# Performance work log

Hardware: AMD Instinct MI355X
Metric: run time of the kernel (lower is better)

Reference implementation:

```python
import jax, jax.numpy as jnp
import numpy as np


def setup_inputs() -> dict:
    key = jax.random.key(0)
    ks = jax.random.split(key, 6)
    B, N, D, Dm, Do = 4, 512, 64, 64, 64
    vertices = jax.random.normal(ks[0], (B, N, D), dtype=jnp.float32)
    mask = jax.random.randint(ks[1], (B, N), 0, 2).astype(bool)
    W_msg = jax.random.normal(ks[2], (Dm, 2 * D), dtype=jnp.float32) / np.sqrt(2 * D).astype(np.float32)
    b_msg = jnp.zeros((Dm,), dtype=jnp.float32)
    W_node = jax.random.normal(ks[3], (Do, D + Dm), dtype=jnp.float32) / np.sqrt(D + Dm).astype(np.float32)
    b_node = jnp.zeros((Do,), dtype=jnp.float32)
    return {"vertices": vertices, "mask": mask, "W_msg": W_msg, "b_msg": b_msg,
            "W_node": W_node, "b_node": b_node}


def reference(vertices, mask, W_msg, b_msg, W_node, b_node):
    # vertices: (B,N,D); mask: (B,N) bool
    D = vertices.shape[-1]
    # message_layer(cat(v_i, v_j)) == v_i @ Wi^T + v_j @ Wj^T + b  (split weight)
    Wi, Wj = W_msg[:, :D], W_msg[:, D:]
    a = jnp.einsum('bnd,md->bnm', vertices, Wi)   # (B,N,Dm) src-half
    c = jnp.einsum('bnd,md->bnm', vertices, Wj)   # (B,N,Dm) dst-half
    msg = jax.nn.relu(a[:, :, None, :] + c[:, None, :, :] + b_msg)  # (B,N,N,Dm)
    pair_mask = (mask[:, :, None] & mask[:, None, :])[..., None]    # (B,N,N,1)
    msg = jnp.where(pair_mask, msg, jnp.zeros((), msg.dtype))
    agg = msg.sum(axis=2)                                           # (B,N,Dm)
    h = jnp.concatenate([vertices, agg], axis=-1)                   # (B,N,D+Dm)
    out = jax.nn.relu(jnp.einsum('bnd,od->bno', h, W_node) + b_node)
    return out
```

## Files before the change

### kernel.cpp

```cpp
#include <hip/hip_runtime.h>


typedef float v2f __attribute__((ext_vector_type(2)));

__device__ __forceinline__ v2f pk_add(v2f a, v2f b) {
    v2f d;
    asm("v_pk_add_f32 %0, %1, %2" : "=v"(d) : "v"(a), "v"(b));
    return d;
}

__global__ __launch_bounds__(256) void prep3(
    const float* __restrict__ V, const int* __restrict__ mask,
    const float* __restrict__ Wmsg, const float* __restrict__ bmsg,
    const float* __restrict__ Wn, const float* __restrict__ bn,
    float* __restrict__ A, float* __restrict__ C, float* __restrict__ O1)
{
    __shared__ float wm_s[64 * 132];
    __shared__ float wn1_s[64 * 68];
    int tid = threadIdx.x;

#pragma unroll
    for (int k = 0; k < 8; ++k) {
        int f4 = tid + k * 256;
        int mm = f4 >> 5, dd = (f4 & 31) << 2;
        *(float4*)&wm_s[mm * 132 + dd] = ((const float4*)Wmsg)[f4];
    }
#pragma unroll
    for (int k = 0; k < 4; ++k) {
        int f4 = tid + k * 256;
        int oo = f4 >> 4, kk = (f4 & 15) << 2;
        *(float4*)&wn1_s[oo * 68 + kk] = *(const float4*)&Wn[oo * 128 + kk];
    }
    __syncthreads();

    int m  = tid & 63;
    int rq = tid >> 6;
    int row0 = __builtin_amdgcn_readfirstlane(blockIdx.x * 8 + rq * 2);
    const float* v0 = V + row0 * 64;
    const float* v1 = v0 + 64;

    float sa0 = bmsg[m], sa1 = sa0;
    float sc0 = 0.f, sc1 = 0.f;
    float so0 = bn[m], so1 = so0;
#pragma unroll
    for (int d0 = 0; d0 < 64; d0 += 4) {
        float4 wa = *(float4*)&wm_s[m * 132 + d0];
        float4 wc = *(float4*)&wm_s[m * 132 + 64 + d0];
        float4 wo = *(float4*)&wn1_s[m * 68 + d0];
        float4 va = *(const float4*)&v0[d0];
        float4 vb = *(const float4*)&v1[d0];
        sa0 = fmaf(va.x, wa.x, sa0); sa0 = fmaf(va.y, wa.y, sa0);
        sa0 = fmaf(va.z, wa.z, sa0); sa0 = fmaf(va.w, wa.w, sa0);
        sc0 = fmaf(va.x, wc.x, sc0); sc0 = fmaf(va.y, wc.y, sc0);
        sc0 = fmaf(va.z, wc.z, sc0); sc0 = fmaf(va.w, wc.w, sc0);
        so0 = fmaf(va.x, wo.x, so0); so0 = fmaf(va.y, wo.y, so0);
        so0 = fmaf(va.z, wo.z, so0); so0 = fmaf(va.w, wo.w, so0);
        sa1 = fmaf(vb.x, wa.x, sa1); sa1 = fmaf(vb.y, wa.y, sa1);
        sa1 = fmaf(vb.z, wa.z, sa1); sa1 = fmaf(vb.w, wa.w, sa1);
        sc1 = fmaf(vb.x, wc.x, sc1); sc1 = fmaf(vb.y, wc.y, sc1);
        sc1 = fmaf(vb.z, wc.z, sc1); sc1 = fmaf(vb.w, wc.w, sc1);
        so1 = fmaf(vb.x, wo.x, so1); so1 = fmaf(vb.y, wo.y, so1);
        so1 = fmaf(vb.z, wo.z, so1); so1 = fmaf(vb.w, wo.w, so1);
    }
    int mk0 = mask[row0], mk1 = mask[row0 + 1];
    A [row0 * 64 + m]       = sa0;
    A [(row0 + 1) * 64 + m] = sa1;
    C [row0 * 64 + m]       = mk0 ? sc0 : -1e30f;
    C [(row0 + 1) * 64 + m] = mk1 ? sc1 : -1e30f;
    O1[row0 * 64 + m]       = so0;
    O1[(row0 + 1) * 64 + m] = so1;
}

__global__ __launch_bounds__(1024) void agg3(
    const int* __restrict__ mask,
    const float* __restrict__ A, const float* __restrict__ C,
    const float* __restrict__ O1, const float* __restrict__ Wn,
    float* __restrict__ out)
{
    __shared__ float smem[8192];
    __shared__ float wn2_s[64 * 68];
    __shared__ float agg_s[8 * 64];

    int tid = threadIdx.x;
    int m  = tid & 63;
    int jc = tid >> 6;
    int i0 = blockIdx.x * 8;
    int b  = blockIdx.x >> 6;
    const float* cb = C + (size_t)b * 512 * 64;

    {
        int oo = tid >> 4, kk = (tid & 15) << 2;
        *(float4*)&wn2_s[oo * 68 + kk] = *(const float4*)&Wn[oo * 128 + 64 + kk];
    }

    v2f ad[8], acc[8];
#pragma unroll
    for (int r = 0; r < 8; ++r) {
        float a = A[(i0 + r) * 64 + m];
        ad[r]  = (v2f){a, a};
        acc[r] = (v2f){0.f, 0.f};
    }

    for (int j0 = 0; j0 < 512; j0 += 128) {
        __syncthreads();
        const float4* src = (const float4*)(cb + (size_t)j0 * 64);
        float4* dst = (float4*)smem;
        dst[tid]        = src[tid];
        dst[tid + 1024] = src[tid + 1024];
        __syncthreads();
        const float* cbase = smem + jc * 8 * 64 + m;
#pragma unroll
        for (int p = 0; p < 4; ++p) {
            v2f c2 = {cbase[p * 128], cbase[p * 128 + 64]};
#pragma unroll
            for (int r = 0; r < 8; ++r) {
                v2f x = pk_add(ad[r], c2);
                x.x = fmaxf(x.x, 0.f);
                x.y = fmaxf(x.y, 0.f);
                acc[r] = pk_add(acc[r], x);
            }
        }
    }
    __syncthreads();
#pragma unroll
    for (int r = 0; r < 8; ++r)
        smem[jc * 512 + r * 64 + m] = acc[r].x + acc[r].y;
    __syncthreads();

    if (tid < 512) {
        int r = tid >> 6;
        float aggsum = 0.f;
#pragma unroll
        for (int q = 0; q < 16; ++q) aggsum += smem[q * 512 + r * 64 + m];
        agg_s[r * 64 + m] = mask[i0 + r] ? aggsum : 0.f;
    }
    __syncthreads();
    if (tid < 512) {
        int r = tid >> 6;
        float s = O1[(i0 + r) * 64 + m];
#pragma unroll
        for (int k = 0; k < 64; k += 4) {
            float4 h4 = *(float4*)&agg_s[r * 64 + k];
            float4 w4 = *(float4*)&wn2_s[m * 68 + k];
            s = fmaf(h4.x, w4.x, s); s = fmaf(h4.y, w4.y, s);
            s = fmaf(h4.z, w4.z, s); s = fmaf(h4.w, w4.w, s);
        }
        out[(i0 + r) * 64 + m] = fmaxf(s, 0.f);
    }
}

extern "C" void kernel_launch(void* const* d_in, const int* in_sizes, int n_in,
                              void* d_out, int out_size, void* d_ws, size_t ws_size,
                              hipStream_t stream) {
    const float* V    = (const float*)d_in[0];
    const int*   mask = (const int*)d_in[1];
    const float* Wmsg = (const float*)d_in[2];
    const float* bmsg = (const float*)d_in[3];
    const float* Wn   = (const float*)d_in[4];
    const float* bn   = (const float*)d_in[5];
    float* outp = (float*)d_out;

    const int BN = in_sizes[1];
    float* A  = (float*)d_ws;
    float* Cc = A  + (size_t)BN * 64;
    float* O1 = Cc + (size_t)BN * 64;

    prep3<<<dim3(BN / 8), dim3(256),  0, stream>>>(V, mask, Wmsg, bmsg, Wn, bn, A, Cc, O1);
    agg3 <<<dim3(BN / 8), dim3(1024), 0, stream>>>(mask, A, Cc, O1, Wn, outp);
}
```

Measured before the change: 20.70 us.

## Fuse prep and aggregation kernels into one cooperative kernel with grid sync

```diff
diff --git a/kernel.cpp b/kernel.cpp
--- a/kernel.cpp
+++ b/kernel.cpp
@@ -1,4 +1,7 @@
 #include <hip/hip_runtime.h>
+#include <hip/hip_cooperative_groups.h>
+
+namespace cg = cooperative_groups;
 
 
 typedef float v2f __attribute__((ext_vector_type(2)));
@@ -9,106 +12,89 @@
     return d;
 }
 
-__global__ __launch_bounds__(256) void prep3(
+__global__ __launch_bounds__(1024) void fused_graphblock(
     const float* __restrict__ V, const int* __restrict__ mask,
     const float* __restrict__ Wmsg, const float* __restrict__ bmsg,
     const float* __restrict__ Wn, const float* __restrict__ bn,
-    float* __restrict__ A, float* __restrict__ C, float* __restrict__ O1)
+    float* __restrict__ C, float* __restrict__ out)
 {
-    __shared__ float wm_s[64 * 132];
-    __shared__ float wn1_s[64 * 68];
+    __shared__ float buf[12800];
+    __shared__ float a_s[512];
+    __shared__ float agg_s[512];
+
     int tid = threadIdx.x;
+    int i0  = blockIdx.x * 8;
+    int b   = blockIdx.x >> 6;
+
+    float* wm  = buf;
+    float* wn1 = buf + 8448;
 
 #pragma unroll
-    for (int k = 0; k < 8; ++k) {
-        int f4 = tid + k * 256;
+    for (int k = 0; k < 2; ++k) {
+        int f4 = tid + k * 1024;
         int mm = f4 >> 5, dd = (f4 & 31) << 2;
-        *(float4*)&wm_s[mm * 132 + dd] = ((const float4*)Wmsg)[f4];
+        *(float4*)&wm[mm * 132 + dd] = ((const float4*)Wmsg)[f4];
     }
-#pragma unroll
-    for (int k = 0; k < 4; ++k) {
-        int f4 = tid + k * 256;
-        int oo = f4 >> 4, kk = (f4 & 15) << 2;
-        *(float4*)&wn1_s[oo * 68 + kk] = *(const float4*)&Wn[oo * 128 + kk];
+    {
+        int oo = tid >> 4, kk = (tid & 15) << 2;
+        *(float4*)&wn1[oo * 68 + kk] = *(const float4*)&Wn[oo * 128 + kk];
     }
     __syncthreads();
 
-    int m  = tid & 63;
-    int rq = tid >> 6;
-    int row0 = __builtin_amdgcn_readfirstlane(blockIdx.x * 8 + rq * 2);
-    const float* v0 = V + row0 * 64;
-    const float* v1 = v0 + 64;
+    float o1 = 0.f;
+    int   mk = 0;
+    if (tid < 512) {
+        int m = tid & 63;
+        int row = __builtin_amdgcn_readfirstlane(i0 + (tid >> 6));
+        const float* v = V + row * 64;
+        float sa = bmsg[m], sc = 0.f, so = bn[m];
+#pragma unroll
+        for (int d0 = 0; d0 < 64; d0 += 4) {
+            float4 va = *(const float4*)&v[d0];
+            float4 wa = *(float4*)&wm[m * 132 + d0];
+            float4 wc = *(float4*)&wm[m * 132 + 64 + d0];
+            float4 wo = *(float4*)&wn1[m * 68 + d0];
+            sa = fmaf(va.x, wa.x, sa); sa = fmaf(va.y, wa.y, sa);
+            sa = fmaf(va.z, wa.z, sa); sa = fmaf(va.w, wa.w, sa);
+            sc = fmaf(va.x, wc.x, sc); sc = fmaf(va.y, wc.y, sc);
+            sc = fmaf(va.z, wc.z, sc); sc = fmaf(va.w, wc.w, sc);
+            so = fmaf(va.x, wo.x, so); so = fmaf(va.y, wo.y, so);
+            so = fmaf(va.z, wo.z, so); so = fmaf(va.w, wo.w, so);
+        }
+        mk = mask[row];
+        a_s[tid] = sa;
+        C[row * 64 + m] = mk ? sc : -1e30f;
+        o1 = so;
+    }
 
-    float sa0 = bmsg[m], sa1 = sa0;
-    float sc0 = 0.f, sc1 = 0.f;
-    float so0 = bn[m], so1 = so0;
-#pragma unroll
-    for (int d0 = 0; d0 < 64; d0 += 4) {
-        float4 wa = *(float4*)&wm_s[m * 132 + d0];
-        float4 wc = *(float4*)&wm_s[m * 132 + 64 + d0];
-        float4 wo = *(float4*)&wn1_s[m * 68 + d0];
-        float4 va = *(const float4*)&v0[d0];
-        float4 vb = *(const float4*)&v1[d0];
-        sa0 = fmaf(va.x, wa.x, sa0); sa0 = fmaf(va.y, wa.y, sa0);
-        sa0 = fmaf(va.z, wa.z, sa0); sa0 = fmaf(va.w, wa.w, sa0);
-        sc0 = fmaf(va.x, wc.x, sc0); sc0 = fmaf(va.y, wc.y, sc0);
-        sc0 = fmaf(va.z, wc.z, sc0); sc0 = fmaf(va.w, wc.w, sc0);
-        so0 = fmaf(va.x, wo.x, so0); so0 = fmaf(va.y, wo.y, so0);
-        so0 = fmaf(va.z, wo.z, so0); so0 = fmaf(va.w, wo.w, so0);
-        sa1 = fmaf(vb.x, wa.x, sa1); sa1 = fmaf(vb.y, wa.y, sa1);
-        sa1 = fmaf(vb.z, wa.z, sa1); sa1 = fmaf(vb.w, wa.w, sa1);
-        sc1 = fmaf(vb.x, wc.x, sc1); sc1 = fmaf(vb.y, wc.y, sc1);
-        sc1 = fmaf(vb.z, wc.z, sc1); sc1 = fmaf(vb.w, wc.w, sc1);
-        so1 = fmaf(vb.x, wo.x, so1); so1 = fmaf(vb.y, wo.y, so1);
-        so1 = fmaf(vb.z, wo.z, so1); so1 = fmaf(vb.w, wo.w, so1);
+    cg::this_grid().sync();
+
+    float* ctile = buf;
+    float* wn2   = buf + 8448;
+    {
+        int oo = tid >> 4, kk = (tid & 15) << 2;
+        *(float4*)&wn2[oo * 68 + kk] = *(const float4*)&Wn[oo * 128 + 64 + kk];
     }
-    int mk0 = mask[row0], mk1 = mask[row0 + 1];
-    A [row0 * 64 + m]       = sa0;
-    A [(row0 + 1) * 64 + m] = sa1;
-    C [row0 * 64 + m]       = mk0 ? sc0 : -1e30f;
-    C [(row0 + 1) * 64 + m] = mk1 ? sc1 : -1e30f;
-    O1[row0 * 64 + m]       = so0;
-    O1[(row0 + 1) * 64 + m] = so1;
-}
 
-__global__ __launch_bounds__(1024) void agg3(
-    const int* __restrict__ mask,
-    const float* __restrict__ A, const float* __restrict__ C,
-    const float* __restrict__ O1, const float* __restrict__ Wn,
-    float* __restrict__ out)
-{
-    __shared__ float smem[8192];
-    __shared__ float wn2_s[64 * 68];
-    __shared__ float agg_s[8 * 64];
-
-    int tid = threadIdx.x;
     int m  = tid & 63;
     int jc = tid >> 6;
-    int i0 = blockIdx.x * 8;
-    int b  = blockIdx.x >> 6;
-    const float* cb = C + (size_t)b * 512 * 64;
-
-    {
-        int oo = tid >> 4, kk = (tid & 15) << 2;
-        *(float4*)&wn2_s[oo * 68 + kk] = *(const float4*)&Wn[oo * 128 + 64 + kk];
-    }
-
     v2f ad[8], acc[8];
 #pragma unroll
     for (int r = 0; r < 8; ++r) {
-        float a = A[(i0 + r) * 64 + m];
+        float a = a_s[r * 64 + m];
         ad[r]  = (v2f){a, a};
         acc[r] = (v2f){0.f, 0.f};
     }
 
+    const float* cb = C + (size_t)b * 512 * 64;
     for (int j0 = 0; j0 < 512; j0 += 128) {
         __syncthreads();
         const float4* src = (const float4*)(cb + (size_t)j0 * 64);
-        float4* dst = (float4*)smem;
+        float4* dst = (float4*)ctile;
         dst[tid]        = src[tid];
         dst[tid + 1024] = src[tid + 1024];
         __syncthreads();
-        const float* cbase = smem + jc * 8 * 64 + m;
+        const float* cbase = ctile + jc * 512 + m;
 #pragma unroll
         for (int p = 0; p < 4; ++p) {
             v2f c2 = {cbase[p * 128], cbase[p * 128 + 64]};
@@ -124,24 +110,24 @@
     __syncthreads();
 #pragma unroll
     for (int r = 0; r < 8; ++r)
-        smem[jc * 512 + r * 64 + m] = acc[r].x + acc[r].y;
+        ctile[jc * 512 + r * 64 + m] = acc[r].x + acc[r].y;
     __syncthreads();
 
     if (tid < 512) {
         int r = tid >> 6;
         float aggsum = 0.f;
 #pragma unroll
-        for (int q = 0; q < 16; ++q) aggsum += smem[q * 512 + r * 64 + m];
-        agg_s[r * 64 + m] = mask[i0 + r] ? aggsum : 0.f;
+        for (int q = 0; q < 16; ++q) aggsum += ctile[q * 512 + r * 64 + m];
+        agg_s[tid] = mk ? aggsum : 0.f;
     }
     __syncthreads();
     if (tid < 512) {
         int r = tid >> 6;
-        float s = O1[(i0 + r) * 64 + m];
+        float s = o1;
 #pragma unroll
         for (int k = 0; k < 64; k += 4) {
             float4 h4 = *(float4*)&agg_s[r * 64 + k];
-            float4 w4 = *(float4*)&wn2_s[m * 68 + k];
+            float4 w4 = *(float4*)&wn2[m * 68 + k];
             s = fmaf(h4.x, w4.x, s); s = fmaf(h4.y, w4.y, s);
             s = fmaf(h4.z, w4.z, s); s = fmaf(h4.w, w4.w, s);
         }
@@ -161,10 +147,10 @@
     float* outp = (float*)d_out;
 
     const int BN = in_sizes[1];
-    float* A  = (float*)d_ws;
-    float* Cc = A  + (size_t)BN * 64;
-    float* O1 = Cc + (size_t)BN * 64;
+    float* C = (float*)d_ws;
 
-    prep3<<<dim3(BN / 8), dim3(256),  0, stream>>>(V, mask, Wmsg, bmsg, Wn, bn, A, Cc, O1);
-    agg3 <<<dim3(BN / 8), dim3(1024), 0, stream>>>(mask, A, Cc, O1, Wn, outp);
+    void* args[] = { (void*)&V, (void*)&mask, (void*)&Wmsg, (void*)&bmsg,
+                     (void*)&Wn, (void*)&bn, (void*)&C, (void*)&outp };
+    hipLaunchCooperativeKernel((const void*)fused_graphblock,
+                               dim3(BN / 8), dim3(1024), args, 0, stream);
 }
```

Result: slower. 56.27 us (+171.8%).
